# Kernel tuning notes

Measured on AMD Instinct MI355X. Metric: run time of the kernel, lower is better.

Reference implementation:

```python
import jax, jax.numpy as jnp
import numpy as np

B, T, I = 32, 512, 96
H, M, R, K = 256, 6, 16, 16
TASK, SENS = 32, 64
MPG = M // 3  # mechanisms per group
OUT = 64


def setup_inputs() -> dict:
    key = jax.random.key(0)
    ks = jax.random.split(key, 12)
    inp = {
        'x': jax.random.normal(ks[0], (B, T, I), jnp.float32),
        # stacked per-mechanism LowRankRNNCell params
        'W_ip': jax.random.normal(ks[1], (M, H, H), jnp.float32) / np.sqrt(H),
        'b_ip': jnp.zeros((M, H), jnp.float32),
        'U': jax.random.normal(ks[2], (M, H, R), jnp.float32) / np.sqrt(R),
        'Vr': jax.random.normal(ks[3], (M, R, H), jnp.float32) / np.sqrt(H),
        'cell_bias': jnp.zeros((M, H), jnp.float32),
        'W_in_task': 0.01 * jax.random.normal(ks[4], (MPG, TASK, H), jnp.float32),
        'W_in_sensory': 0.01 * jax.random.normal(ks[5], (MPG, SENS, H), jnp.float32),
        'W_Q': 0.01 * jax.random.normal(ks[6], (M, H, K), jnp.float32),
        'W_K': 0.01 * jax.random.normal(ks[7], (M, H, K), jnp.float32),
        'W_V': 0.01 * jax.random.normal(ks[8], (M, H, H), jnp.float32),
        'W_out': jax.random.normal(ks[9], (H * MPG, OUT), jnp.float32) / np.sqrt(H * MPG),
        'b_out': jnp.zeros((OUT,), jnp.float32),
    }
    return inp


def _rim_forward(x, W_ip, b_ip, U, Vr, cell_bias, W_in_task, W_in_sensory,
                 W_Q, W_K, W_V, W_out, b_out):
    scale = jnp.float32(1.0 / np.sqrt(K))

    def step(Hs, x_t):
        # input routing: group 0 <- task input, group 1 <- sensory, group 2 <- zeros
        x_task = x_t[:, -TASK:]
        x_sens = x_t[:, :-TASK]
        g0 = jnp.einsum('bi,mih->bmh', x_task, W_in_task)
        g1 = jnp.einsum('bi,mih->bmh', x_sens, W_in_sensory)
        A_in = jnp.concatenate([g0, g1, jnp.zeros_like(g0)], axis=1)  # [B,M,H]
        # batched LowRankRNNCell update per mechanism
        inp_part = jnp.einsum('bmi,mih->bmh', A_in, W_ip) + b_ip
        rec = jnp.einsum('bmr,mrh->bmh', jnp.einsum('bmh,mhr->bmr', Hs, U), Vr)
        H_in = jnp.tanh(inp_part + rec + cell_bias)  # [B,M,H]
        # communication attention (exact einsum structure of the original)
        Qc = jnp.einsum('bmh,mhk->bmk', H_in, W_Q)
        Kc = jnp.einsum('bmh,mhk->bmk', H_in, W_K)
        Vc = jnp.einsum('bmh,mhj->bjm', H_in, W_V)  # V_comm[b,h,m]
        attn = jax.nn.softmax(jnp.einsum('bmk,bnk->bmn', Qc, Kc) * scale, axis=-1)
        A_comm = jnp.einsum('bmn,bhm->bnh', attn, Vc)
        H_new = H_in + A_comm
        out = H_new[:, -MPG:].reshape(H_new.shape[0], -1) @ W_out + b_out
        return H_new, (out, H_new, A_in, A_comm, attn)

    H0 = jnp.zeros((x.shape[0], M, H), x.dtype)
    _, (outs, Hseq, Ain_seq, Acomm_seq, attn_seq) = jax.lax.scan(
        step, H0, jnp.swapaxes(x, 0, 1))
    # time-major -> batch-major where the torch code stacks on dim=1 (outputs)
    outputs = jnp.swapaxes(outs, 0, 1)  # [B,T,OUT]
    return outputs, Hseq, Ain_seq, Acomm_seq, attn_seq


def reference(x, W_ip, b_ip, U, Vr, cell_bias, W_in_task, W_in_sensory,
              W_Q, W_K, W_V, W_out, b_out):
    return _rim_forward(x, W_ip, b_ip, U, Vr, cell_bias, W_in_task,
                        W_in_sensory, W_Q, W_K, W_V, W_out, b_out)
```

## Files before the change

### kernel.cpp

```cpp
#include <hip/hip_runtime.h>
#include <math.h>

#define BB 32
#define TT 512
#define II 96
#define HH 256
#define MM 6
#define OUTD 64

#define O_HSEQ  1048576
#define O_AIN   26214400
#define O_ACM   51380224
#define O_ATTN  76546048

#define WS_WEFF 0
#define WS_UT   49152
#define WS_WQT  73728
#define WS_WKT  98304
#define WS_VCH  122880
#define WS_QK   319488
#define WS_FLAG 331776
#define WS_COOP_FLOATS 333824

#define LBAR() asm volatile("s_waitcnt lgkmcnt(0)\n\ts_barrier" ::: "memory")

__global__ __launch_bounds__(256) void rim_weff(
    const float* __restrict__ Wtask, const float* __restrict__ Wsens,
    const float* __restrict__ Wip,
    const float* __restrict__ U, const float* __restrict__ WQ, const float* __restrict__ WK,
    float* __restrict__ Weff, float* __restrict__ Ut, float* __restrict__ WQt, float* __restrict__ WKt)
{
  __shared__ float row[256];
  const int bidx = blockIdx.x;
  const int tid = threadIdx.x;
  if (bidx < 192) {
    int m, i;
    if (bidx < 32)       { m = 0; i = bidx; }
    else if (bidx < 64)  { m = 1; i = bidx - 32; }
    else if (bidx < 128) { m = 2; i = bidx - 64; }
    else                 { m = 3; i = bidx - 128; }
    row[tid] = (m < 2) ? Wtask[(m * 32 + i) * 256 + tid]
                       : Wsens[((m - 2) * 64 + i) * 256 + tid];
    __syncthreads();
    float acc = 0.f;
    const float* wip = Wip + m * 65536 + tid;
    #pragma unroll 8
    for (int j = 0; j < 256; ++j) acc += row[j] * wip[j * 256];
    const int base = (m == 0) ? 0 : (m == 1) ? 8192 : (m == 2) ? 16384 : 32768;
    Weff[base + i * 256 + tid] = acc;
  } else {
    const int p = bidx - 192;
    const int m = p >> 4, r = p & 15;
    Ut [(m * 16 + r) * 256 + tid] = U [m * 4096 + tid * 16 + r];
    WQt[(m * 16 + r) * 256 + tid] = WQ[m * 4096 + tid * 16 + r];
    WKt[(m * 16 + r) * 256 + tid] = WK[m * 4096 + tid * 16 + r];
  }
}

__global__ __launch_bounds__(256) void rim_pre(
    const float* __restrict__ x,
    const float* __restrict__ Wtask, const float* __restrict__ Wsens,
    float* __restrict__ Ain)
{
  __shared__ float xr[16][96];
  const int tid = threadIdx.x;
  const int rb0 = blockIdx.x * 16;
  for (int idx = tid; idx < 16 * 96; idx += 256) {
    int r = idx / 96, c = idx % 96;
    int rb = rb0 + r; int t = rb >> 5, b = rb & 31;
    xr[r][c] = x[(b * TT + t) * II + c];
  }
  __syncthreads();
  const int h = tid;
  float acc[16];

  for (int m = 0; m < 4; ++m) {
    const int cnt  = (m < 2) ? 32 : 64;
    const int xoff = (m < 2) ? 64 : 0;
    const float* W = (m < 2) ? (Wtask + m * 32 * 256) : (Wsens + (m - 2) * 64 * 256);
    #pragma unroll
    for (int r = 0; r < 16; ++r) acc[r] = 0.f;
    for (int i = 0; i < cnt; ++i) {
      float w = W[i * 256 + h];
      #pragma unroll
      for (int r = 0; r < 16; ++r) acc[r] += xr[r][xoff + i] * w;
    }
    #pragma unroll
    for (int r = 0; r < 16; ++r) {
      int rb = rb0 + r; int t = rb >> 5, b = rb & 31;
      Ain[((t * 32 + b) * 6 + m) * 256 + h] = acc[r];
    }
  }
  #pragma unroll
  for (int r = 0; r < 16; ++r) {
    int rb = rb0 + r; int t = rb >> 5, b = rb & 31;
    Ain[((t * 32 + b) * 6 + 4) * 256 + h] = 0.f;
    Ain[((t * 32 + b) * 6 + 5) * 256 + h] = 0.f;
  }
}

__global__ __launch_bounds__(512, 2) void rim_step(
    const float* __restrict__ x,
    const float* __restrict__ Vr, const float* __restrict__ WV,
    const float* __restrict__ bip, const float* __restrict__ cbias,
    const float* __restrict__ UtW, const float* __restrict__ WQtW,
    const float* __restrict__ WKtW, const float* __restrict__ WeffW,
    float* __restrict__ VcHG, float* __restrict__ QKG,
    unsigned int* __restrict__ seqG,
    float* __restrict__ Hseq, float* __restrict__ Acm, float* __restrict__ attnO)
{
  __shared__ __align__(16) float Hl[256];
  __shared__ __align__(16) float Hin[256];
  __shared__ float biasl[256];
  __shared__ float Utl[16][257];
  __shared__ float Vrl[16][257];
  __shared__ float WQtl[16][257];
  __shared__ float WKtl[16][257];
  __shared__ float Weffl[64][256];
  __shared__ float inpl[2][256];
  __shared__ float xl[2][96];
  __shared__ float tmpUr[16];
  __shared__ float qklw[4][192];

  const int bid = blockIdx.x;
  const int m = bid >> 5;
  const int b = bid & 31;
  const int tid = threadIdx.x;
  const int g32 = tid >> 5, l32 = tid & 31;
  const int h_out = tid & 255, p = tid >> 8;
  const int g16 = tid >> 4, l16 = tid & 15;
  const int w64 = tid >> 6, lane = tid & 63;

  const int base = (m == 0) ? 0 : (m == 1) ? 8192 : (m == 2) ? 16384 : 32768;
  const int cnt  = (m < 2) ? 32 : 64;
  const int xoff = (m < 2) ? 64 : 0;

  for (int i = tid; i < 4096; i += 512) {
    int r = i >> 8, c = i & 255;
    Utl [r][c] = UtW [m * 4096 + i];
    Vrl [r][c] = Vr  [m * 4096 + i];
    WQtl[r][c] = WQtW[m * 4096 + i];
    WKtl[r][c] = WKtW[m * 4096 + i];
  }
  if (m < 4)
    for (int i = tid; i < cnt * 256; i += 512)
      ((float*)Weffl)[i] = WeffW[base + i];
  if (tid < 256) {
    biasl[tid] = bip[m * 256 + tid] + cbias[m * 256 + tid];
    Hl[tid] = 0.f;
  }
  float xreg = 0.f;
  if (m < 4 && tid < 96) {
    xl[0][tid] = x[((size_t)b * TT + 0) * II + tid];
    xreg       = x[((size_t)b * TT + 1) * II + tid];
  }
  float w[128];
  #pragma unroll
  for (int j = 0; j < 128; ++j)
    w[j] = WV[((size_t)(m * 256 + p * 128 + j)) * 256 + h_out];
  __syncthreads();
  if (m < 4 && tid < 256) {
    float a = 0.f;
    for (int i = 0; i < cnt; ++i) a += xl[0][xoff + i] * Weffl[i][tid];
    inpl[0][tid] = a;
  }
  __syncthreads();

  for (int t = 0; t < TT; ++t) {
    const int buf = t & 1;
    const int mb12 = (buf * 32 + b) * 12;
    const int qb   = (buf * 32 + b) * 192;
    const unsigned target = (unsigned)(t + 1);

    if (m < 4 && tid < 96) {
      xl[(t + 1) & 1][tid] = xreg;
      xreg = (t + 2 < TT) ? x[((size_t)b * TT + t + 2) * II + tid] : 0.f;
    }

    {
      float s = 0.f;
      const float* up = &Utl[g32][0];
      #pragma unroll
      for (int h = l32; h < 256; h += 32) s += Hl[h] * up[h];
      #pragma unroll
      for (int off = 16; off > 0; off >>= 1) s += __shfl_down(s, off, 32);
      if (l32 == 0) tmpUr[g32] = s;
    }
    LBAR();

    if (tid < 256) {
      float rec = 0.f;
      #pragma unroll
      for (int r = 0; r < 16; ++r) rec += tmpUr[r] * Vrl[r][tid];
      float inp = (m < 4) ? inpl[buf][tid] : 0.f;
      Hin[tid] = tanhf(inp + rec + biasl[tid]);
    }
    LBAR();

    {
      const int r = g16 & 15;
      const float* wp = (g16 < 16) ? &WQtl[r][0] : &WKtl[r][0];
      float s = 0.f;
      #pragma unroll
      for (int j = 0; j < 16; ++j) { int h = l16 + 16 * j; s += Hin[h] * wp[h]; }
      s += __shfl_down(s, 8, 16);
      s += __shfl_down(s, 4, 16);
      s += __shfl_down(s, 2, 16);
      s += __shfl_down(s, 1, 16);
      if (l16 == 0)
        __hip_atomic_store(&QKG[qb + ((g16 < 16) ? 0 : 96) + m * 16 + r], s,
                           __ATOMIC_RELAXED, __HIP_MEMORY_SCOPE_SYSTEM);
    }
    float accVc = 0.f;
    {
      const float4* h4 = (const float4*)&Hin[p * 128];
      #pragma unroll
      for (int q = 0; q < 32; ++q) {
        float4 hv = h4[q];
        accVc += hv.x * w[4 * q] + hv.y * w[4 * q + 1]
               + hv.z * w[4 * q + 2] + hv.w * w[4 * q + 3];
      }
      __hip_atomic_store(&VcHG[(mb12 + m * 2 + p) * 256 + h_out], accVc,
                         __ATOMIC_RELAXED, __HIP_MEMORY_SCOPE_SYSTEM);
    }
    asm volatile("s_waitcnt vmcnt(0)" ::: "memory");
    if (lane == 0)
      __hip_atomic_store(&seqG[b * 64 + m * 8 + w64], target,
                         __ATOMIC_RELAXED, __HIP_MEMORY_SCOPE_SYSTEM);

    if (w64 < 4) {
      if (lane < 48) {
        while (__hip_atomic_load(&seqG[b * 64 + lane],
                                 __ATOMIC_RELAXED, __HIP_MEMORY_SCOPE_SYSTEM)
               < target) { }
      }
      float q0 = __hip_atomic_load(&QKG[qb + lane],       __ATOMIC_RELAXED, __HIP_MEMORY_SCOPE_SYSTEM);
      float q1 = __hip_atomic_load(&QKG[qb + 64 + lane],  __ATOMIC_RELAXED, __HIP_MEMORY_SCOPE_SYSTEM);
      float q2 = __hip_atomic_load(&QKG[qb + 128 + lane], __ATOMIC_RELAXED, __HIP_MEMORY_SCOPE_SYSTEM);
      float vA[6], vB[6];
      #pragma unroll
      for (int mm = 0; mm < 6; ++mm) {
        if (mm != m)
          vA[mm] = __hip_atomic_load(&VcHG[(mb12 + mm * 2 + 0) * 256 + h_out],
                                     __ATOMIC_RELAXED, __HIP_MEMORY_SCOPE_SYSTEM);
        vB[mm] = __hip_atomic_load(&VcHG[(mb12 + mm * 2 + 1) * 256 + h_out],
                                   __ATOMIC_RELAXED, __HIP_MEMORY_SCOPE_SYSTEM);
      }
      vA[m] = accVc;

      qklw[w64][lane]       = q0;
      qklw[w64][64 + lane]  = q1;
      qklw[w64][128 + lane] = q2;

      float a = 0.f;
      {
        const int mm6 = (lane < 36) ? (lane / 6) : 0;
        const int nn  = (lane < 36) ? (lane % 6) : 0;
        if (lane < 36) {
          const float* qw = &qklw[w64][mm6 * 16];
          const float* kw = &qklw[w64][96 + nn * 16];
          float s = 0.f;
          #pragma unroll
          for (int k = 0; k < 16; ++k) s += qw[k] * kw[k];
          s *= 0.25f;
          float mx = s;
          #pragma unroll
          for (int d = 1; d < 6; ++d)
            mx = fmaxf(mx, __shfl(s, mm6 * 6 + ((nn + d) % 6), 64));
          float e = __expf(s - mx);
          float sm = e;
          #pragma unroll
          for (int d = 1; d < 6; ++d)
            sm += __shfl(e, mm6 * 6 + ((nn + d) % 6), 64);
          a = e / sm;
        }
      }
      if (m == 0 && w64 == 0 && lane < 36)
        attnO[((size_t)t * 32 + b) * 36 + lane] = a;

      float ac = 0.f;
      #pragma unroll
      for (int mm = 0; mm < 6; ++mm) {
        float amm = __shfl(a, mm * 6 + m, 64);
        ac += amm * (vA[mm] + vB[mm]);
      }
      float hn = Hin[tid] + ac;
      Hl[tid] = hn;
      size_t gi = (((size_t)t * 32 + b) * 6 + m) * 256 + tid;
      Hseq[gi] = hn;
      Acm[gi]  = ac;
    } else {
      if (m < 4) {
        const int h = tid - 256, nb = (t + 1) & 1;
        float a = 0.f;
        for (int i = 0; i < cnt; ++i) a += xl[nb][xoff + i] * Weffl[i][h];
        inpl[nb][h] = a;
      }
    }
    LBAR();
  }
}

__global__ __launch_bounds__(256) void rim_out(
    const float* __restrict__ Hseq, const float* __restrict__ Wout,
    const float* __restrict__ bout, float* __restrict__ out0)
{
  __shared__ float hrow[4][512];
  const int tid = threadIdx.x;
  const int row0 = blockIdx.x * 4;
  for (int i = tid; i < 4 * 512; i += 256) {
    int r = i >> 9, j = i & 511;
    int rb = row0 + r; int b = rb >> 9, t = rb & 511;
    hrow[r][j] = Hseq[((size_t)(t * 32 + b) * 6 + 4 + (j >> 8)) * 256 + (j & 255)];
  }
  __syncthreads();
  const int r = tid >> 6, o = tid & 63;
  const int rb = row0 + r;
  float s = bout[o];
  const float* hp = hrow[r];
  const float* wp = Wout + o;
  #pragma unroll 8
  for (int j = 0; j < 512; ++j) s += hp[j] * wp[(size_t)j * 64];
  out0[(size_t)rb * 64 + o] = s;
}

__global__ __launch_bounds__(512) void rim_loop(
    const float* __restrict__ x,
    const float* __restrict__ Vr, const float* __restrict__ WV,
    const float* __restrict__ Wout, const float* __restrict__ bout,
    const float* __restrict__ bip, const float* __restrict__ cbias,
    const float* __restrict__ Ut, const float* __restrict__ WQt, const float* __restrict__ WKt,
    const float* __restrict__ Weff,
    float* __restrict__ out0, float* __restrict__ Hseq,
    float* __restrict__ Acm, float* __restrict__ attnO)
{
  __shared__ float Hl[6][256];
  __shared__ float Hin[6][256];
  __shared__ float biasl[6][256];
  __shared__ float Vcp[2][6][256];
  __shared__ float tmpUr[6][16];
  __shared__ float Qc[6][16], Kc[6][16];
  __shared__ float attnl[36];
  __shared__ float pout[8][64];
  __shared__ float xl[96];
  __shared__ float inpl[4][256];

  const int b = blockIdx.x;
  const int tid = threadIdx.x;
  const int wid = tid >> 5, lane = tid & 31;

  for (int i = tid; i < 1536; i += 512) {
    int m = i >> 8, h = i & 255;
    biasl[m][h] = bip[i] + cbias[i];
    Hl[m][h] = 0.f;
  }
  __syncthreads();

  for (int t = 0; t < TT; ++t) {
    if (tid < 96) xl[tid] = x[(b * TT + t) * II + tid];
    __syncthreads();
    for (int mh = tid; mh < 1024; mh += 512) {
      int m = mh >> 8, h = mh & 255;
      const int base = (m == 0) ? 0 : (m == 1) ? 8192 : (m == 2) ? 16384 : 32768;
      const int cnt  = (m < 2) ? 32 : 64;
      const int xoff = (m < 2) ? 64 : 0;
      float a = 0.f;
      for (int i = 0; i < cnt; ++i) a += xl[xoff + i] * Weff[base + i * 256 + h];
      inpl[m][h] = a;
    }

    for (int pq = wid; pq < 96; pq += 16) {
      int m = pq >> 4, r = pq & 15;
      const float* up = Ut + (m * 16 + r) * 256;
      float s = 0.f;
      #pragma unroll
      for (int h = lane; h < 256; h += 32) s += Hl[m][h] * up[h];
// ... 68 lines not shown
      #pragma unroll
      for (int m = 0; m < 6; ++m)
        ac += attnl[m * 6 + n] * (Vcp[0][m][h] + Vcp[1][m][h]);
      float hn = Hin[n][h] + ac;
      Hl[n][h] = hn;
      size_t gi = ((size_t)(t * 32 + b) * 6 + n) * 256 + h;
      Hseq[gi] = hn;
      Acm[gi]  = ac;
    }
    __syncthreads();

    {
      const int o = tid & 63, js = tid >> 6;
      const float* hp = &Hl[4][0];
      const float* wp = Wout + (size_t)(js * 64) * 64 + o;
      float s = 0.f;
      #pragma unroll 8
      for (int jj = 0; jj < 64; ++jj) s += hp[js * 64 + jj] * wp[(size_t)jj * 64];
      pout[js][o] = s;
    }
    __syncthreads();
    if (tid < 64) {
      float s = bout[tid];
      #pragma unroll
      for (int js = 0; js < 8; ++js) s += pout[js][tid];
      out0[(size_t)(b * TT + t) * 64 + tid] = s;
    }
  }
}

extern "C" void kernel_launch(void* const* d_in, const int* in_sizes, int n_in,
                              void* d_out, int out_size, void* d_ws, size_t ws_size,
                              hipStream_t stream) {
  const float* x    = (const float*)d_in[0];
  const float* W_ip = (const float*)d_in[1];
  const float* b_ip = (const float*)d_in[2];
  const float* U    = (const float*)d_in[3];
  const float* Vr   = (const float*)d_in[4];
  const float* cb   = (const float*)d_in[5];
  const float* Wt   = (const float*)d_in[6];
  const float* Wsn  = (const float*)d_in[7];
  const float* WQ   = (const float*)d_in[8];
  const float* WK   = (const float*)d_in[9];
  const float* WV   = (const float*)d_in[10];
  const float* Wo   = (const float*)d_in[11];
  const float* bo   = (const float*)d_in[12];

  float* out  = (float*)d_out;
  float* Hseq = out + O_HSEQ;
  float* Ain  = out + O_AIN;
  float* Acm  = out + O_ACM;
  float* attn = out + O_ATTN;

  float* ws   = (float*)d_ws;
  float* Weff = ws + WS_WEFF;
  float* Ut   = ws + WS_UT;
  float* WQt  = ws + WS_WQT;
  float* WKt  = ws + WS_WKT;

  hipLaunchKernelGGL(rim_weff, dim3(288), dim3(256), 0, stream,
                     Wt, Wsn, W_ip, U, WQ, WK, Weff, Ut, WQt, WKt);
  hipLaunchKernelGGL(rim_pre, dim3(1024), dim3(256), 0, stream,
                     x, Wt, Wsn, Ain);

  if (ws_size >= (size_t)WS_COOP_FLOATS * sizeof(float)) {
    float* VcHG = ws + WS_VCH;
    float* QKG  = ws + WS_QK;
    unsigned int* seqG = (unsigned int*)(ws + WS_FLAG);
    hipMemsetAsync((void*)seqG, 0, 2048 * sizeof(unsigned int), stream);

    void* args[] = { (void*)&x, (void*)&Vr, (void*)&WV, (void*)&b_ip, (void*)&cb,
                     (void*)&Ut, (void*)&WQt, (void*)&WKt, (void*)&Weff,
                     (void*)&VcHG, (void*)&QKG, (void*)&seqG,
                     (void*)&Hseq, (void*)&Acm, (void*)&attn };
    hipLaunchCooperativeKernel((void*)rim_step, dim3(192), dim3(512), args, 0, stream);

    hipLaunchKernelGGL(rim_out, dim3(4096), dim3(256), 0, stream,
                       Hseq, Wo, bo, out);
  } else {
    hipLaunchKernelGGL(rim_loop, dim3(32), dim3(512), 0, stream,
                       x, Vr, WV, Wo, bo, b_ip, cb, Ut, WQt, WKt, Weff,
                       out, Hseq, Acm, attn);
  }
}
```

Baseline: 3.162 ms.

## Replace per-step flag barrier with tagged value exchange and fuse weight prep

Inter-block communication in the cooperative recurrent kernel now packs each value with its timestep tag into a 64-bit word. Consumers spin directly on the data instead of on a separate sequence-flag array after a vmcnt drain. The Vc partial sums are combined in LDS before publishing, and a dedicated wavefront computes the softmax once per block. The Weff and transposed-weight precompute kernel is folded into the step kernel's prologue, removing one launch but making every block redo the W_ip product. The aim is shorter per-timestep synchronization latency, at the cost of doubled exchange traffic and a heavier prologue.

```diff
diff --git a/kernel.cpp b/kernel.cpp
--- a/kernel.cpp
+++ b/kernel.cpp
@@ -1,28 +1,320 @@
 #include <hip/hip_runtime.h>
 #include <math.h>
+
+typedef unsigned long long u64;
 
 #define BB 32
 #define TT 512
 #define II 96
-#define HH 256
-#define MM 6
-#define OUTD 64
 
 #define O_HSEQ  1048576
 #define O_AIN   26214400
 #define O_ACM   51380224
 #define O_ATTN  76546048
 
-#define WS_WEFF 0
-#define WS_UT   49152
-#define WS_WQT  73728
-#define WS_WKT  98304
-#define WS_VCH  122880
-#define WS_QK   319488
-#define WS_FLAG 331776
-#define WS_COOP_FLOATS 333824
+#define WS_VCF  0
+#define WS_QKT  196608
+#define WS_COOP_FLOATS 221184
+#define WS_F_WEFF 0
+#define WS_F_UT   49152
+#define WS_F_WQT  73728
+#define WS_F_WKT  98304
+#define WS_F_FLOATS 122880
 
 #define LBAR() asm volatile("s_waitcnt lgkmcnt(0)\n\ts_barrier" ::: "memory")
+
+__device__ __forceinline__ u64 sysld(const u64* p) {
+  return __hip_atomic_load(p, __ATOMIC_RELAXED, __HIP_MEMORY_SCOPE_SYSTEM);
+}
+__device__ __forceinline__ void sysst(u64* p, u64 v) {
+  __hip_atomic_store(p, v, __ATOMIC_RELAXED, __HIP_MEMORY_SCOPE_SYSTEM);
+}
+__device__ __forceinline__ u64 packtv(unsigned tag, float v) {
+  return ((u64)tag << 32) | (u64)__float_as_uint(v);
+}
+
+__global__ __launch_bounds__(256) void rim_pre(
+    const float* __restrict__ x,
+    const float* __restrict__ Wtask, const float* __restrict__ Wsens,
+    float* __restrict__ Ain)
+{
+  __shared__ float xr[16][96];
+  const int tid = threadIdx.x;
+  const int rb0 = blockIdx.x * 16;
+  for (int idx = tid; idx < 16 * 96; idx += 256) {
+    int r = idx / 96, c = idx % 96;
+    int rb = rb0 + r; int t = rb >> 5, b = rb & 31;
+    xr[r][c] = x[(b * TT + t) * II + c];
+  }
+  __syncthreads();
+  const int h = tid;
+  float acc[16];
+
+  for (int m = 0; m < 4; ++m) {
+    const int cnt  = (m < 2) ? 32 : 64;
+    const int xoff = (m < 2) ? 64 : 0;
+    const float* W = (m < 2) ? (Wtask + m * 32 * 256) : (Wsens + (m - 2) * 64 * 256);
+    #pragma unroll
+    for (int r = 0; r < 16; ++r) acc[r] = 0.f;
+    for (int i = 0; i < cnt; ++i) {
+      float w = W[i * 256 + h];
+      #pragma unroll
+      for (int r = 0; r < 16; ++r) acc[r] += xr[r][xoff + i] * w;
+    }
+    #pragma unroll
+    for (int r = 0; r < 16; ++r) {
+      int rb = rb0 + r; int t = rb >> 5, b = rb & 31;
+      Ain[((t * 32 + b) * 6 + m) * 256 + h] = acc[r];
+    }
+  }
+  #pragma unroll
+  for (int r = 0; r < 16; ++r) {
+    int rb = rb0 + r; int t = rb >> 5, b = rb & 31;
+    Ain[((t * 32 + b) * 6 + 4) * 256 + h] = 0.f;
+    Ain[((t * 32 + b) * 6 + 5) * 256 + h] = 0.f;
+  }
+}
+
+__global__ __launch_bounds__(512, 1) void rim_step(
+    const float* __restrict__ x,
+    const float* __restrict__ U, const float* __restrict__ Vr,
+    const float* __restrict__ WV,
+    const float* __restrict__ bip, const float* __restrict__ cbias,
+    const float* __restrict__ WQ, const float* __restrict__ WK,
+    const float* __restrict__ Wtask, const float* __restrict__ Wsens,
+    const float* __restrict__ Wip,
+    u64* __restrict__ VCF, u64* __restrict__ QKT,
+    float* __restrict__ Hseq, float* __restrict__ Acm, float* __restrict__ attnO)
+{
+  __shared__ __align__(16) float Hl[256];
+  __shared__ __align__(16) float Hin[256];
+  __shared__ float biasl[256];
+  __shared__ float Utl[16][257];
+  __shared__ float Vrl[16][257];
+  __shared__ float WQtl[16][257];
+  __shared__ float WKtl[16][257];
+  __shared__ float Weffl[64][256];
+  __shared__ float inpl[2][256];
+  __shared__ float xl[2][96];
+  __shared__ float Vcp1[256];
+  __shared__ float tmpUr[16];
+  __shared__ float attnl[40];
+  __shared__ float qkl[192];
+  __shared__ float wtmp[16][256];
+
+  const int bid = blockIdx.x;
+  const int m = bid >> 5;
+  const int b = bid & 31;
+  const int tid = threadIdx.x;
+  const int g32 = tid >> 5, l32 = tid & 31;
+  const int h_out = tid & 255, p = tid >> 8;
+  const int g16 = tid >> 4, l16 = tid & 15;
+  const int w64 = tid >> 6, lane = tid & 63;
+
+  const int cnt  = (m < 2) ? 32 : 64;
+  const int xoff = (m < 2) ? 64 : 0;
+
+  for (int i = tid; i < 4096; i += 512) {
+    int r = i >> 8, c = i & 255;
+    Utl [r][c] = U [m * 4096 + c * 16 + r];
+    WQtl[r][c] = WQ[m * 4096 + c * 16 + r];
+    WKtl[r][c] = WK[m * 4096 + c * 16 + r];
+    Vrl [r][c] = Vr[m * 4096 + i];
+  }
+  if (tid < 256) {
+    biasl[tid] = bip[m * 256 + tid] + cbias[m * 256 + tid];
+    Hl[tid] = 0.f;
+  }
+  float xreg = 0.f;
+  if (m < 4 && tid < 96) {
+    xl[0][tid] = x[((size_t)b * TT + 0) * II + tid];
+    xreg       = x[((size_t)b * TT + 1) * II + tid];
+  }
+  float w[128];
+  #pragma unroll
+  for (int j = 0; j < 128; ++j)
+    w[j] = WV[((size_t)(m * 256 + p * 128 + j)) * 256 + h_out];
+
+  if (m < 4) {
+    const float* Win = (m < 2) ? (Wtask + m * 32 * 256) : (Wsens + (m - 2) * 64 * 256);
+    const float* wip = Wip + m * 65536;
+    const int hh = tid & 255, half8 = (tid >> 8) * 8;
+    for (int c0 = 0; c0 < cnt; c0 += 16) {
+      __syncthreads();
+      for (int i = tid; i < 16 * 256; i += 512)
+        wtmp[i >> 8][i & 255] = Win[(c0 + (i >> 8)) * 256 + (i & 255)];
+      __syncthreads();
+      float acc8[8];
+      #pragma unroll
+      for (int r = 0; r < 8; ++r) acc8[r] = 0.f;
+      for (int j = 0; j < 256; ++j) {
+        float wv = wip[j * 256 + hh];
+        #pragma unroll
+        for (int r = 0; r < 8; ++r) acc8[r] += wtmp[half8 + r][j] * wv;
+      }
+      #pragma unroll
+      for (int r = 0; r < 8; ++r) Weffl[c0 + half8 + r][hh] = acc8[r];
+    }
+  }
+  __syncthreads();
+  if (m < 4 && tid < 256) {
+    float a = 0.f;
+    for (int i = 0; i < cnt; ++i) a += xl[0][xoff + i] * Weffl[i][tid];
+    inpl[0][tid] = a;
+  }
+  __syncthreads();
+
+  for (int t = 0; t < TT; ++t) {
+    const int buf = t & 1;
+    const unsigned target = (unsigned)(t + 1);
+    u64* vcb = VCF + (size_t)(buf * 32 + b) * 1536;
+    u64* qkb = QKT + (size_t)(buf * 32 + b) * 192;
+
+    if (m < 4 && tid < 96) {
+      xl[(t + 1) & 1][tid] = xreg;
+      xreg = (t + 2 < TT) ? x[((size_t)b * TT + t + 2) * II + tid] : 0.f;
+    }
+
+    {
+      float s = 0.f;
+      const float* up = &Utl[g32][0];
+      #pragma unroll
+      for (int h = l32; h < 256; h += 32) s += Hl[h] * up[h];
+      #pragma unroll
+      for (int off = 16; off > 0; off >>= 1) s += __shfl_down(s, off, 32);
+      if (l32 == 0) tmpUr[g32] = s;
+    }
+    LBAR();
+
+    if (tid < 256) {
+      float rec = 0.f;
+      #pragma unroll
+      for (int r = 0; r < 16; ++r) rec += tmpUr[r] * Vrl[r][tid];
+      float inp = (m < 4) ? inpl[buf][tid] : 0.f;
+      Hin[tid] = tanhf(inp + rec + biasl[tid]);
+    }
+    LBAR();
+
+    {
+      const int r = g16 & 15;
+      const float* wp = (g16 < 16) ? &WQtl[r][0] : &WKtl[r][0];
+      float s = 0.f;
+      #pragma unroll
+      for (int j = 0; j < 16; ++j) { int h = l16 + 16 * j; s += Hin[h] * wp[h]; }
+      s += __shfl_down(s, 8, 16);
+      s += __shfl_down(s, 4, 16);
+      s += __shfl_down(s, 2, 16);
+      s += __shfl_down(s, 1, 16);
+      if (l16 == 0)
+        sysst(&qkb[((g16 < 16) ? 0 : 96) + m * 16 + r], packtv(target, s));
+    }
+    float accVc = 0.f;
+    {
+      const float4* h4 = (const float4*)&Hin[p * 128];
+      #pragma unroll
+      for (int q = 0; q < 32; ++q) {
+        float4 hv = h4[q];
+        accVc += hv.x * w[4 * q] + hv.y * w[4 * q + 1]
+               + hv.z * w[4 * q + 2] + hv.w * w[4 * q + 3];
+      }
+    }
+    if (p == 1) Vcp1[h_out] = accVc;
+    LBAR();
+
+    float vC[6];
+    if (tid < 256) {
+      float vown = accVc + Vcp1[tid];
+      sysst(&vcb[m * 256 + tid], packtv(target, vown));
+      u64 vw[6];
+      #pragma unroll
+      for (int mm = 0; mm < 6; ++mm)
+        if (mm != m) vw[mm] = sysld(&vcb[mm * 256 + tid]);
+      #pragma unroll
+      for (int mm = 0; mm < 6; ++mm)
+        if (mm != m)
+          while ((unsigned)(vw[mm] >> 32) != target)
+            vw[mm] = sysld(&vcb[mm * 256 + tid]);
+      #pragma unroll
+      for (int mm = 0; mm < 6; ++mm)
+        vC[mm] = (mm == m) ? vown : __uint_as_float((unsigned)vw[mm]);
+    } else if (w64 == 7) {
+      u64 a0 = sysld(&qkb[lane]);
+      u64 a1 = sysld(&qkb[64 + lane]);
+      u64 a2 = sysld(&qkb[128 + lane]);
+      while ((unsigned)(a0 >> 32) != target) a0 = sysld(&qkb[lane]);
+      while ((unsigned)(a1 >> 32) != target) a1 = sysld(&qkb[64 + lane]);
+      while ((unsigned)(a2 >> 32) != target) a2 = sysld(&qkb[128 + lane]);
+      qkl[lane]       = __uint_as_float((unsigned)a0);
+      qkl[64 + lane]  = __uint_as_float((unsigned)a1);
+      qkl[128 + lane] = __uint_as_float((unsigned)a2);
+      asm volatile("s_waitcnt lgkmcnt(0)" ::: "memory");
+      if (lane < 36) {
+        const int mm6 = lane / 6, nn = lane % 6;
+        float s = 0.f;
+        #pragma unroll
+        for (int k = 0; k < 16; ++k) s += qkl[mm6 * 16 + k] * qkl[96 + nn * 16 + k];
+        s *= 0.25f;
+        float mx = s;
+        #pragma unroll
+        for (int d = 1; d < 6; ++d)
+          mx = fmaxf(mx, __shfl(s, mm6 * 6 + ((nn + d) % 6), 64));
+        float e = __expf(s - mx);
+        float sm = e;
+        #pragma unroll
+        for (int d = 1; d < 6; ++d)
+          sm += __shfl(e, mm6 * 6 + ((nn + d) % 6), 64);
+        float a = e / sm;
+        attnl[lane] = a;
+        if (m == 0) attnO[((size_t)t * 32 + b) * 36 + lane] = a;
+      }
+    } else {
+      if (m < 4) {
+        const int nb = (t + 1) & 1;
+        for (int h = tid - 256; h < 256; h += 192) {
+          float a = 0.f;
+          for (int i = 0; i < cnt; ++i) a += xl[nb][xoff + i] * Weffl[i][h];
+          inpl[nb][h] = a;
+        }
+      }
+    }
+    LBAR();
+
+    if (tid < 256) {
+      float ac = 0.f;
+      #pragma unroll
+      for (int mm = 0; mm < 6; ++mm) ac += attnl[mm * 6 + m] * vC[mm];
+      float hn = Hin[tid] + ac;
+      Hl[tid] = hn;
+      size_t gi = (((size_t)t * 32 + b) * 6 + m) * 256 + tid;
+      Hseq[gi] = hn;
+      Acm[gi]  = ac;
+    }
+    LBAR();
+  }
+}
+
+__global__ __launch_bounds__(256) void rim_out(
+    const float* __restrict__ Hseq, const float* __restrict__ Wout,
+    const float* __restrict__ bout, float* __restrict__ out0)
+{
+  __shared__ float hrow[4][512];
+  const int tid = threadIdx.x;
+  const int row0 = blockIdx.x * 4;
+  for (int i = tid; i < 4 * 512; i += 256) {
+    int r = i >> 9, j = i & 511;
+    int rb = row0 + r; int b = rb >> 9, t = rb & 511;
+    hrow[r][j] = Hseq[((size_t)(t * 32 + b) * 6 + 4 + (j >> 8)) * 256 + (j & 255)];
+  }
+  __syncthreads();
+  const int r = tid >> 6, o = tid & 63;
+  const int rb = row0 + r;
+  float s = bout[o];
+  const float* hp = hrow[r];
+  const float* wp = Wout + o;
+  #pragma unroll 8
+  for (int j = 0; j < 512; ++j) s += hp[j] * wp[(size_t)j * 64];
+  out0[(size_t)rb * 64 + o] = s;
+}
 
 __global__ __launch_bounds__(256) void rim_weff(
     const float* __restrict__ Wtask, const float* __restrict__ Wsens,
@@ -55,273 +347,6 @@
     WQt[(m * 16 + r) * 256 + tid] = WQ[m * 4096 + tid * 16 + r];
     WKt[(m * 16 + r) * 256 + tid] = WK[m * 4096 + tid * 16 + r];
   }
-}
-
-__global__ __launch_bounds__(256) void rim_pre(
-    const float* __restrict__ x,
-    const float* __restrict__ Wtask, const float* __restrict__ Wsens,
-    float* __restrict__ Ain)
-{
-  __shared__ float xr[16][96];
-  const int tid = threadIdx.x;
-  const int rb0 = blockIdx.x * 16;
-  for (int idx = tid; idx < 16 * 96; idx += 256) {
-    int r = idx / 96, c = idx % 96;
-    int rb = rb0 + r; int t = rb >> 5, b = rb & 31;
-    xr[r][c] = x[(b * TT + t) * II + c];
-  }
-  __syncthreads();
-  const int h = tid;
-  float acc[16];
-
-  for (int m = 0; m < 4; ++m) {
-    const int cnt  = (m < 2) ? 32 : 64;
-    const int xoff = (m < 2) ? 64 : 0;
-    const float* W = (m < 2) ? (Wtask + m * 32 * 256) : (Wsens + (m - 2) * 64 * 256);
-    #pragma unroll
-    for (int r = 0; r < 16; ++r) acc[r] = 0.f;
-    for (int i = 0; i < cnt; ++i) {
-      float w = W[i * 256 + h];
-      #pragma unroll
-      for (int r = 0; r < 16; ++r) acc[r] += xr[r][xoff + i] * w;
-    }
-    #pragma unroll
-    for (int r = 0; r < 16; ++r) {
-      int rb = rb0 + r; int t = rb >> 5, b = rb & 31;
-      Ain[((t * 32 + b) * 6 + m) * 256 + h] = acc[r];
-    }
-  }
-  #pragma unroll
-  for (int r = 0; r < 16; ++r) {
-    int rb = rb0 + r; int t = rb >> 5, b = rb & 31;
-    Ain[((t * 32 + b) * 6 + 4) * 256 + h] = 0.f;
-    Ain[((t * 32 + b) * 6 + 5) * 256 + h] = 0.f;
-  }
-}
-
-__global__ __launch_bounds__(512, 2) void rim_step(
-    const float* __restrict__ x,
-    const float* __restrict__ Vr, const float* __restrict__ WV,
-    const float* __restrict__ bip, const float* __restrict__ cbias,
-    const float* __restrict__ UtW, const float* __restrict__ WQtW,
-    const float* __restrict__ WKtW, const float* __restrict__ WeffW,
-    float* __restrict__ VcHG, float* __restrict__ QKG,
-    unsigned int* __restrict__ seqG,
-    float* __restrict__ Hseq, float* __restrict__ Acm, float* __restrict__ attnO)
-{
-  __shared__ __align__(16) float Hl[256];
-  __shared__ __align__(16) float Hin[256];
-  __shared__ float biasl[256];
-  __shared__ float Utl[16][257];
-  __shared__ float Vrl[16][257];
-  __shared__ float WQtl[16][257];
-  __shared__ float WKtl[16][257];
-  __shared__ float Weffl[64][256];
-  __shared__ float inpl[2][256];
-  __shared__ float xl[2][96];
-  __shared__ float tmpUr[16];
-  __shared__ float qklw[4][192];
-
-  const int bid = blockIdx.x;
-  const int m = bid >> 5;
-  const int b = bid & 31;
-  const int tid = threadIdx.x;
-  const int g32 = tid >> 5, l32 = tid & 31;
-  const int h_out = tid & 255, p = tid >> 8;
-  const int g16 = tid >> 4, l16 = tid & 15;
-  const int w64 = tid >> 6, lane = tid & 63;
-
-  const int base = (m == 0) ? 0 : (m == 1) ? 8192 : (m == 2) ? 16384 : 32768;
-  const int cnt  = (m < 2) ? 32 : 64;
-  const int xoff = (m < 2) ? 64 : 0;
-
-  for (int i = tid; i < 4096; i += 512) {
-    int r = i >> 8, c = i & 255;
-    Utl [r][c] = UtW [m * 4096 + i];
-    Vrl [r][c] = Vr  [m * 4096 + i];
-    WQtl[r][c] = WQtW[m * 4096 + i];
-    WKtl[r][c] = WKtW[m * 4096 + i];
-  }
-  if (m < 4)
-    for (int i = tid; i < cnt * 256; i += 512)
-      ((float*)Weffl)[i] = WeffW[base + i];
-  if (tid < 256) {
-    biasl[tid] = bip[m * 256 + tid] + cbias[m * 256 + tid];
-    Hl[tid] = 0.f;
-  }
-  float xreg = 0.f;
-  if (m < 4 && tid < 96) {
-    xl[0][tid] = x[((size_t)b * TT + 0) * II + tid];
-    xreg       = x[((size_t)b * TT + 1) * II + tid];
-  }
-  float w[128];
-  #pragma unroll
-  for (int j = 0; j < 128; ++j)
-    w[j] = WV[((size_t)(m * 256 + p * 128 + j)) * 256 + h_out];
-  __syncthreads();
-  if (m < 4 && tid < 256) {
-    float a = 0.f;
-    for (int i = 0; i < cnt; ++i) a += xl[0][xoff + i] * Weffl[i][tid];
-    inpl[0][tid] = a;
-  }
-  __syncthreads();
-
-  for (int t = 0; t < TT; ++t) {
-    const int buf = t & 1;
-    const int mb12 = (buf * 32 + b) * 12;
-    const int qb   = (buf * 32 + b) * 192;
-    const unsigned target = (unsigned)(t + 1);
-
-    if (m < 4 && tid < 96) {
-      xl[(t + 1) & 1][tid] = xreg;
-      xreg = (t + 2 < TT) ? x[((size_t)b * TT + t + 2) * II + tid] : 0.f;
-    }
-
-    {
-      float s = 0.f;
-      const float* up = &Utl[g32][0];
-      #pragma unroll
-      for (int h = l32; h < 256; h += 32) s += Hl[h] * up[h];
-      #pragma unroll
-      for (int off = 16; off > 0; off >>= 1) s += __shfl_down(s, off, 32);
-      if (l32 == 0) tmpUr[g32] = s;
-    }
-    LBAR();
-
-    if (tid < 256) {
-      float rec = 0.f;
-      #pragma unroll
-      for (int r = 0; r < 16; ++r) rec += tmpUr[r] * Vrl[r][tid];
-      float inp = (m < 4) ? inpl[buf][tid] : 0.f;
-      Hin[tid] = tanhf(inp + rec + biasl[tid]);
-    }
-    LBAR();
-
-    {
-      const int r = g16 & 15;
-      const float* wp = (g16 < 16) ? &WQtl[r][0] : &WKtl[r][0];
-      float s = 0.f;
-      #pragma unroll
-      for (int j = 0; j < 16; ++j) { int h = l16 + 16 * j; s += Hin[h] * wp[h]; }
-      s += __shfl_down(s, 8, 16);
-      s += __shfl_down(s, 4, 16);
-      s += __shfl_down(s, 2, 16);
-      s += __shfl_down(s, 1, 16);
-      if (l16 == 0)
-        __hip_atomic_store(&QKG[qb + ((g16 < 16) ? 0 : 96) + m * 16 + r], s,
-                           __ATOMIC_RELAXED, __HIP_MEMORY_SCOPE_SYSTEM);
-    }
-    float accVc = 0.f;
-    {
-      const float4* h4 = (const float4*)&Hin[p * 128];
-      #pragma unroll
-      for (int q = 0; q < 32; ++q) {
-        float4 hv = h4[q];
-        accVc += hv.x * w[4 * q] + hv.y * w[4 * q + 1]
-               + hv.z * w[4 * q + 2] + hv.w * w[4 * q + 3];
-      }
-      __hip_atomic_store(&VcHG[(mb12 + m * 2 + p) * 256 + h_out], accVc,
-                         __ATOMIC_RELAXED, __HIP_MEMORY_SCOPE_SYSTEM);
-    }
-    asm volatile("s_waitcnt vmcnt(0)" ::: "memory");
-    if (lane == 0)
-      __hip_atomic_store(&seqG[b * 64 + m * 8 + w64], target,
-                         __ATOMIC_RELAXED, __HIP_MEMORY_SCOPE_SYSTEM);
-
-    if (w64 < 4) {
-      if (lane < 48) {
-        while (__hip_atomic_load(&seqG[b * 64 + lane],
-                                 __ATOMIC_RELAXED, __HIP_MEMORY_SCOPE_SYSTEM)
-               < target) { }
-      }
-      float q0 = __hip_atomic_load(&QKG[qb + lane],       __ATOMIC_RELAXED, __HIP_MEMORY_SCOPE_SYSTEM);
-      float q1 = __hip_atomic_load(&QKG[qb + 64 + lane],  __ATOMIC_RELAXED, __HIP_MEMORY_SCOPE_SYSTEM);
-      float q2 = __hip_atomic_load(&QKG[qb + 128 + lane], __ATOMIC_RELAXED, __HIP_MEMORY_SCOPE_SYSTEM);
-      float vA[6], vB[6];
-      #pragma unroll
-      for (int mm = 0; mm < 6; ++mm) {
-        if (mm != m)
-          vA[mm] = __hip_atomic_load(&VcHG[(mb12 + mm * 2 + 0) * 256 + h_out],
-                                     __ATOMIC_RELAXED, __HIP_MEMORY_SCOPE_SYSTEM);
-        vB[mm] = __hip_atomic_load(&VcHG[(mb12 + mm * 2 + 1) * 256 + h_out],
-                                   __ATOMIC_RELAXED, __HIP_MEMORY_SCOPE_SYSTEM);
-      }
-      vA[m] = accVc;
-
-      qklw[w64][lane]       = q0;
-      qklw[w64][64 + lane]  = q1;
-      qklw[w64][128 + lane] = q2;
-
-      float a = 0.f;
-      {
-        const int mm6 = (lane < 36) ? (lane / 6) : 0;
-        const int nn  = (lane < 36) ? (lane % 6) : 0;
-        if (lane < 36) {
-          const float* qw = &qklw[w64][mm6 * 16];
-          const float* kw = &qklw[w64][96 + nn * 16];
-          float s = 0.f;
-          #pragma unroll
-          for (int k = 0; k < 16; ++k) s += qw[k] * kw[k];
-          s *= 0.25f;
-          float mx = s;
-          #pragma unroll
-          for (int d = 1; d < 6; ++d)
-            mx = fmaxf(mx, __shfl(s, mm6 * 6 + ((nn + d) % 6), 64));
-          float e = __expf(s - mx);
-          float sm = e;
-          #pragma unroll
-          for (int d = 1; d < 6; ++d)
-            sm += __shfl(e, mm6 * 6 + ((nn + d) % 6), 64);
-          a = e / sm;
-        }
-      }
-      if (m == 0 && w64 == 0 && lane < 36)
-        attnO[((size_t)t * 32 + b) * 36 + lane] = a;
-
-      float ac = 0.f;
-      #pragma unroll
-      for (int mm = 0; mm < 6; ++mm) {
-        float amm = __shfl(a, mm * 6 + m, 64);
-        ac += amm * (vA[mm] + vB[mm]);
-      }
-      float hn = Hin[tid] + ac;
-      Hl[tid] = hn;
-      size_t gi = (((size_t)t * 32 + b) * 6 + m) * 256 + tid;
-      Hseq[gi] = hn;
-      Acm[gi]  = ac;
-    } else {
-      if (m < 4) {
-        const int h = tid - 256, nb = (t + 1) & 1;
-        float a = 0.f;
-        for (int i = 0; i < cnt; ++i) a += xl[nb][xoff + i] * Weffl[i][h];
-        inpl[nb][h] = a;
-      }
-    }
-    LBAR();
-  }
-}
-
-__global__ __launch_bounds__(256) void rim_out(
-    const float* __restrict__ Hseq, const float* __restrict__ Wout,
-    const float* __restrict__ bout, float* __restrict__ out0)
-{
-  __shared__ float hrow[4][512];
-  const int tid = threadIdx.x;
-  const int row0 = blockIdx.x * 4;
-  for (int i = tid; i < 4 * 512; i += 256) {
-    int r = i >> 9, j = i & 511;
-    int rb = row0 + r; int b = rb >> 9, t = rb & 511;
-    hrow[r][j] = Hseq[((size_t)(t * 32 + b) * 6 + 4 + (j >> 8)) * 256 + (j & 255)];
-  }
-  __syncthreads();
-  const int r = tid >> 6, o = tid & 63;
-  const int rb = row0 + r;
-  float s = bout[o];
-  const float* hp = hrow[r];
-  const float* wp = Wout + o;
-  #pragma unroll 8
-  for (int j = 0; j < 512; ++j) s += hp[j] * wp[(size_t)j * 64];
-  out0[(size_t)rb * 64 + o] = s;
 }
 
 __global__ __launch_bounds__(512) void rim_loop(
@@ -496,32 +521,32 @@
   float* Acm  = out + O_ACM;
   float* attn = out + O_ATTN;
 
-  float* ws   = (float*)d_ws;
-  float* Weff = ws + WS_WEFF;
-  float* Ut   = ws + WS_UT;
-  float* WQt  = ws + WS_WQT;
-  float* WKt  = ws + WS_WKT;
-
-  hipLaunchKernelGGL(rim_weff, dim3(288), dim3(256), 0, stream,
-                     Wt, Wsn, W_ip, U, WQ, WK, Weff, Ut, WQt, WKt);
+  float* ws = (float*)d_ws;
+
   hipLaunchKernelGGL(rim_pre, dim3(1024), dim3(256), 0, stream,
                      x, Wt, Wsn, Ain);
 
   if (ws_size >= (size_t)WS_COOP_FLOATS * sizeof(float)) {
-    float* VcHG = ws + WS_VCH;
-    float* QKG  = ws + WS_QK;
-    unsigned int* seqG = (unsigned int*)(ws + WS_FLAG);
-    hipMemsetAsync((void*)seqG, 0, 2048 * sizeof(unsigned int), stream);
-
-    void* args[] = { (void*)&x, (void*)&Vr, (void*)&WV, (void*)&b_ip, (void*)&cb,
-                     (void*)&Ut, (void*)&WQt, (void*)&WKt, (void*)&Weff,
-                     (void*)&VcHG, (void*)&QKG, (void*)&seqG,
+    u64* VCF = (u64*)(ws + WS_VCF);
+    u64* QKT = (u64*)(ws + WS_QKT);
+    hipMemsetAsync((void*)ws, 0, (size_t)WS_COOP_FLOATS * sizeof(float), stream);
+
+    void* args[] = { (void*)&x, (void*)&U, (void*)&Vr, (void*)&WV,
+                     (void*)&b_ip, (void*)&cb, (void*)&WQ, (void*)&WK,
+                     (void*)&Wt, (void*)&Wsn, (void*)&W_ip,
+                     (void*)&VCF, (void*)&QKT,
                      (void*)&Hseq, (void*)&Acm, (void*)&attn };
     hipLaunchCooperativeKernel((void*)rim_step, dim3(192), dim3(512), args, 0, stream);
 
     hipLaunchKernelGGL(rim_out, dim3(4096), dim3(256), 0, stream,
                        Hseq, Wo, bo, out);
   } else {
+    float* Weff = ws + WS_F_WEFF;
+    float* Ut   = ws + WS_F_UT;
+    float* WQt  = ws + WS_F_WQT;
+    float* WKt  = ws + WS_F_WKT;
+    hipLaunchKernelGGL(rim_weff, dim3(288), dim3(256), 0, stream,
+                       Wt, Wsn, W_ip, U, WQ, WK, Weff, Ut, WQt, WKt);
     hipLaunchKernelGGL(rim_loop, dim3(32), dim3(512), 0, stream,
                        x, Vr, WV, Wo, bo, b_ip, cb, Ut, WQt, WKt, Weff,
                        out, Hseq, Acm, attn);
```

After: 3.966 ms. 25.4% more time.

## Batch four sequences per block in cooperative RIM step kernel

Applied to the files above, without the earlier changes.

Each block of the cooperative recurrent kernel now handles one mechanism for four batch elements instead of one, shrinking the grid from 192 to 48 blocks. The two halves of the V projection are summed locally before publishing, which halves cross-block Vc traffic. Cross-block flag synchronization drops to one flag per block and six pollers per step. The trade-off is that each block runs four serialized sub-steps with extra barriers per timestep and uses fewer CUs, in exchange for cheaper inter-block synchronization.

```diff
diff --git a/kernel.cpp b/kernel.cpp
--- a/kernel.cpp
+++ b/kernel.cpp
@@ -4,9 +4,6 @@
 #define BB 32
 #define TT 512
 #define II 96
-#define HH 256
-#define MM 6
-#define OUTD 64
 
 #define O_HSEQ  1048576
 #define O_AIN   26214400
@@ -17,12 +14,25 @@
 #define WS_UT   49152
 #define WS_WQT  73728
 #define WS_WKT  98304
-#define WS_VCH  122880
-#define WS_QK   319488
-#define WS_FLAG 331776
-#define WS_COOP_FLOATS 333824
+#define WS_VC   122880
+#define WS_QK   221184
+#define WS_FLAG 233472
+#define WS_COOP_FLOATS 233728
 
 #define LBAR() asm volatile("s_waitcnt lgkmcnt(0)\n\ts_barrier" ::: "memory")
+
+__device__ __forceinline__ float sysldf(const float* p) {
+  return __hip_atomic_load(p, __ATOMIC_RELAXED, __HIP_MEMORY_SCOPE_SYSTEM);
+}
+__device__ __forceinline__ void sysstf(float* p, float v) {
+  __hip_atomic_store(p, v, __ATOMIC_RELAXED, __HIP_MEMORY_SCOPE_SYSTEM);
+}
+__device__ __forceinline__ unsigned sysld32(const unsigned* p) {
+  return __hip_atomic_load(p, __ATOMIC_RELAXED, __HIP_MEMORY_SCOPE_SYSTEM);
+}
+__device__ __forceinline__ void sysst32(unsigned* p, unsigned v) {
+  __hip_atomic_store(p, v, __ATOMIC_RELAXED, __HIP_MEMORY_SCOPE_SYSTEM);
+}
 
 __global__ __launch_bounds__(256) void rim_weff(
     const float* __restrict__ Wtask, const float* __restrict__ Wsens,
@@ -105,35 +115,38 @@
     const float* __restrict__ bip, const float* __restrict__ cbias,
     const float* __restrict__ UtW, const float* __restrict__ WQtW,
     const float* __restrict__ WKtW, const float* __restrict__ WeffW,
-    float* __restrict__ VcHG, float* __restrict__ QKG,
-    unsigned int* __restrict__ seqG,
+    float* __restrict__ VcG, float* __restrict__ QKG,
+    unsigned* __restrict__ seqG,
     float* __restrict__ Hseq, float* __restrict__ Acm, float* __restrict__ attnO)
 {
-  __shared__ __align__(16) float Hl[256];
-  __shared__ __align__(16) float Hin[256];
+  __shared__ float Hl[4][256];
+  __shared__ float Hin[4][256];
+  __shared__ float inpl[4][2][256];
+  __shared__ float xl[4][2][96];
+  __shared__ float qkl[4][192];
+  __shared__ float attnl[4][40];
   __shared__ float biasl[256];
-  __shared__ float Utl[16][257];
-  __shared__ float Vrl[16][257];
+  __shared__ float Vcp1[256];
+  __shared__ float tmpUr[16];
+  __shared__ float Utl[16][256];
+  __shared__ float Vrl[16][256];
   __shared__ float WQtl[16][257];
   __shared__ float WKtl[16][257];
   __shared__ float Weffl[64][256];
-  __shared__ float inpl[2][256];
-  __shared__ float xl[2][96];
-  __shared__ float tmpUr[16];
-  __shared__ float qklw[4][192];
 
   const int bid = blockIdx.x;
-  const int m = bid >> 5;
-  const int b = bid & 31;
+  const int m  = bid >> 3;
+  const int g  = bid & 7;
+  const int b0 = g * 4;
   const int tid = threadIdx.x;
   const int g32 = tid >> 5, l32 = tid & 31;
-  const int h_out = tid & 255, p = tid >> 8;
   const int g16 = tid >> 4, l16 = tid & 15;
   const int w64 = tid >> 6, lane = tid & 63;
-
-  const int base = (m == 0) ? 0 : (m == 1) ? 8192 : (m == 2) ? 16384 : 32768;
+  const int h_out = tid & 255, p = tid >> 8;
+
   const int cnt  = (m < 2) ? 32 : 64;
   const int xoff = (m < 2) ? 64 : 0;
+  const int wbase = (m == 0) ? 0 : (m == 1) ? 8192 : (m == 2) ? 16384 : 32768;
 
   for (int i = tid; i < 4096; i += 512) {
     int r = i >> 8, c = i & 255;
@@ -144,15 +157,15 @@
   }
   if (m < 4)
     for (int i = tid; i < cnt * 256; i += 512)
-      ((float*)Weffl)[i] = WeffW[base + i];
-  if (tid < 256) {
-    biasl[tid] = bip[m * 256 + tid] + cbias[m * 256 + tid];
-    Hl[tid] = 0.f;
-  }
+      ((float*)Weffl)[i] = WeffW[wbase + i];
+  if (tid < 256) biasl[tid] = bip[m * 256 + tid] + cbias[m * 256 + tid];
+  for (int i = tid; i < 1024; i += 512) Hl[i >> 8][i & 255] = 0.f;
+
   float xreg = 0.f;
-  if (m < 4 && tid < 96) {
-    xl[0][tid] = x[((size_t)b * TT + 0) * II + tid];
-    xreg       = x[((size_t)b * TT + 1) * II + tid];
+  if (m < 4 && tid < 384) {
+    const int bi = tid / 96, c = tid % 96;
+    xl[bi][0][c] = x[((size_t)(b0 + bi) * TT + 0) * II + c];
+    xreg         = x[((size_t)(b0 + bi) * TT + 1) * II + c];
   }
   float w[128];
   #pragma unroll
@@ -160,141 +173,153 @@
     w[j] = WV[((size_t)(m * 256 + p * 128 + j)) * 256 + h_out];
   __syncthreads();
   if (m < 4 && tid < 256) {
-    float a = 0.f;
-    for (int i = 0; i < cnt; ++i) a += xl[0][xoff + i] * Weffl[i][tid];
-    inpl[0][tid] = a;
+    #pragma unroll
+    for (int bi = 0; bi < 4; ++bi) {
+      float a = 0.f;
+      for (int i = 0; i < cnt; ++i) a += xl[bi][0][xoff + i] * Weffl[i][tid];
+      inpl[bi][0][tid] = a;
+    }
   }
   __syncthreads();
 
+  float accVcS[4];
   for (int t = 0; t < TT; ++t) {
-    const int buf = t & 1;
-    const int mb12 = (buf * 32 + b) * 12;
-    const int qb   = (buf * 32 + b) * 192;
+    const int buf = t & 1, nb = buf ^ 1;
     const unsigned target = (unsigned)(t + 1);
-
-    if (m < 4 && tid < 96) {
-      xl[(t + 1) & 1][tid] = xreg;
-      xreg = (t + 2 < TT) ? x[((size_t)b * TT + t + 2) * II + tid] : 0.f;
-    }
-
-    {
+    const int vcbase = (buf * 32 + b0) * 1536;
+    const int qkbase = (buf * 32 + b0) * 192;
+
+    if (m < 4 && tid < 384) {
+      const int bi = tid / 96, c = tid % 96;
+      xl[bi][nb][c] = xreg;
+      xreg = (t + 2 < TT) ? x[((size_t)(b0 + bi) * TT + t + 2) * II + c] : 0.f;
+    }
+
+    #pragma unroll
+    for (int bi = 0; bi < 4; ++bi) {
+      if (bi > 0 && tid < 256)
+        sysstf(&VcG[vcbase + (bi - 1) * 1536 + m * 256 + tid],
+               accVcS[bi - 1] + Vcp1[tid]);
+      {
+        float s = 0.f;
+        const float* up = &Utl[g32][0];
+        const float* hp = &Hl[bi][0];
+        #pragma unroll
+        for (int h = l32; h < 256; h += 32) s += hp[h] * up[h];
+        #pragma unroll
+        for (int off = 16; off; off >>= 1) s += __shfl_down(s, off, 32);
+        if (l32 == 0) tmpUr[g32] = s;
+      }
+      LBAR();
+      if (tid < 256) {
+        float rec = 0.f;
+        #pragma unroll
+        for (int r = 0; r < 16; ++r) rec += tmpUr[r] * Vrl[r][tid];
+        float inp = (m < 4) ? inpl[bi][buf][tid] : 0.f;
+        Hin[bi][tid] = tanhf(inp + rec + biasl[tid]);
+      }
+      LBAR();
+      {
+        const int r = g16 & 15;
+        const float* wp = (g16 < 16) ? &WQtl[r][0] : &WKtl[r][0];
+        const float* hp = &Hin[bi][0];
+        float s = 0.f;
+        #pragma unroll
+        for (int j = 0; j < 16; ++j) { int h = l16 + 16 * j; s += hp[h] * wp[h]; }
+        s += __shfl_down(s, 8, 16);
+        s += __shfl_down(s, 4, 16);
+        s += __shfl_down(s, 2, 16);
+        s += __shfl_down(s, 1, 16);
+        if (l16 == 0)
+          sysstf(&QKG[qkbase + bi * 192 + ((g16 < 16) ? 0 : 96) + m * 16 + r], s);
+      }
+      {
+        float acc = 0.f;
+        const float4* h4 = (const float4*)&Hin[bi][p * 128];
+        #pragma unroll
+        for (int q = 0; q < 32; ++q) {
+          float4 hv = h4[q];
+          acc += hv.x * w[4 * q] + hv.y * w[4 * q + 1]
+               + hv.z * w[4 * q + 2] + hv.w * w[4 * q + 3];
+        }
+        accVcS[bi] = acc;
+        if (p == 1) Vcp1[h_out] = acc;
+      }
+      LBAR();
+    }
+    if (tid < 256)
+      sysstf(&VcG[vcbase + 3 * 1536 + m * 256 + tid], accVcS[3] + Vcp1[tid]);
+
+    asm volatile("s_waitcnt vmcnt(0)" ::: "memory");
+    LBAR();
+    if (tid == 0) sysst32(&seqG[m * 8 + g], target);
+    if (w64 == 0 && lane < 6)
+      while (sysld32(&seqG[lane * 8 + g]) < target) { }
+    LBAR();
+
+    float vA[4][6];
+    if (tid < 256) {
+      #pragma unroll
+      for (int bi = 0; bi < 4; ++bi)
+        #pragma unroll
+        for (int mm = 0; mm < 6; ++mm)
+          vA[bi][mm] = sysldf(&VcG[vcbase + bi * 1536 + mm * 256 + tid]);
+    } else {
+      const int f0 = (tid - 256) * 3;
+      float q0 = sysldf(&QKG[qkbase + f0]);
+      float q1 = sysldf(&QKG[qkbase + f0 + 1]);
+      float q2 = sysldf(&QKG[qkbase + f0 + 2]);
+      if (m < 4) {
+        const int h = tid - 256;
+        #pragma unroll
+        for (int bi = 0; bi < 4; ++bi) {
+          float a = 0.f;
+          for (int i = 0; i < cnt; ++i) a += xl[bi][nb][xoff + i] * Weffl[i][h];
+          inpl[bi][nb][h] = a;
+        }
+      }
+      ((float*)qkl)[f0]     = q0;
+      ((float*)qkl)[f0 + 1] = q1;
+      ((float*)qkl)[f0 + 2] = q2;
+    }
+    LBAR();
+
+    if (w64 >= 4 && lane < 36) {
+      const int bi = w64 - 4;
+      const int mm6 = lane / 6, nn = lane % 6;
+      const float* qw = &qkl[bi][mm6 * 16];
+      const float* kw = &qkl[bi][96 + nn * 16];
       float s = 0.f;
-      const float* up = &Utl[g32][0];
-      #pragma unroll
-      for (int h = l32; h < 256; h += 32) s += Hl[h] * up[h];
-      #pragma unroll
-      for (int off = 16; off > 0; off >>= 1) s += __shfl_down(s, off, 32);
-      if (l32 == 0) tmpUr[g32] = s;
+      #pragma unroll
+      for (int k = 0; k < 16; ++k) s += qw[k] * kw[k];
+      s *= 0.25f;
+      float mx = s;
+      #pragma unroll
+      for (int d = 1; d < 6; ++d)
+        mx = fmaxf(mx, __shfl(s, mm6 * 6 + ((nn + d) % 6), 64));
+      float e = __expf(s - mx);
+      float sm = e;
+      #pragma unroll
+      for (int d = 1; d < 6; ++d)
+        sm += __shfl(e, mm6 * 6 + ((nn + d) % 6), 64);
+      float a = e / sm;
+      attnl[bi][lane] = a;
+      if (m == 0) attnO[((size_t)t * 32 + (b0 + bi)) * 36 + lane] = a;
     }
     LBAR();
 
     if (tid < 256) {
-      float rec = 0.f;
-      #pragma unroll
-      for (int r = 0; r < 16; ++r) rec += tmpUr[r] * Vrl[r][tid];
-      float inp = (m < 4) ? inpl[buf][tid] : 0.f;
-      Hin[tid] = tanhf(inp + rec + biasl[tid]);
-    }
-    LBAR();
-
-    {
-      const int r = g16 & 15;
-      const float* wp = (g16 < 16) ? &WQtl[r][0] : &WKtl[r][0];
-      float s = 0.f;
-      #pragma unroll
-      for (int j = 0; j < 16; ++j) { int h = l16 + 16 * j; s += Hin[h] * wp[h]; }
-      s += __shfl_down(s, 8, 16);
-      s += __shfl_down(s, 4, 16);
-      s += __shfl_down(s, 2, 16);
-      s += __shfl_down(s, 1, 16);
-      if (l16 == 0)
-        __hip_atomic_store(&QKG[qb + ((g16 < 16) ? 0 : 96) + m * 16 + r], s,
-                           __ATOMIC_RELAXED, __HIP_MEMORY_SCOPE_SYSTEM);
-    }
-    float accVc = 0.f;
-    {
-      const float4* h4 = (const float4*)&Hin[p * 128];
-      #pragma unroll
-      for (int q = 0; q < 32; ++q) {
-        float4 hv = h4[q];
-        accVc += hv.x * w[4 * q] + hv.y * w[4 * q + 1]
-               + hv.z * w[4 * q + 2] + hv.w * w[4 * q + 3];
-      }
-      __hip_atomic_store(&VcHG[(mb12 + m * 2 + p) * 256 + h_out], accVc,
-                         __ATOMIC_RELAXED, __HIP_MEMORY_SCOPE_SYSTEM);
-    }
-    asm volatile("s_waitcnt vmcnt(0)" ::: "memory");
-    if (lane == 0)
-      __hip_atomic_store(&seqG[b * 64 + m * 8 + w64], target,
-                         __ATOMIC_RELAXED, __HIP_MEMORY_SCOPE_SYSTEM);
-
-    if (w64 < 4) {
-      if (lane < 48) {
-        while (__hip_atomic_load(&seqG[b * 64 + lane],
-                                 __ATOMIC_RELAXED, __HIP_MEMORY_SCOPE_SYSTEM)
-               < target) { }
-      }
-      float q0 = __hip_atomic_load(&QKG[qb + lane],       __ATOMIC_RELAXED, __HIP_MEMORY_SCOPE_SYSTEM);
-      float q1 = __hip_atomic_load(&QKG[qb + 64 + lane],  __ATOMIC_RELAXED, __HIP_MEMORY_SCOPE_SYSTEM);
-      float q2 = __hip_atomic_load(&QKG[qb + 128 + lane], __ATOMIC_RELAXED, __HIP_MEMORY_SCOPE_SYSTEM);
-      float vA[6], vB[6];
-      #pragma unroll
-      for (int mm = 0; mm < 6; ++mm) {
-        if (mm != m)
-          vA[mm] = __hip_atomic_load(&VcHG[(mb12 + mm * 2 + 0) * 256 + h_out],
-                                     __ATOMIC_RELAXED, __HIP_MEMORY_SCOPE_SYSTEM);
-        vB[mm] = __hip_atomic_load(&VcHG[(mb12 + mm * 2 + 1) * 256 + h_out],
-                                   __ATOMIC_RELAXED, __HIP_MEMORY_SCOPE_SYSTEM);
-      }
-      vA[m] = accVc;
-
-      qklw[w64][lane]       = q0;
-      qklw[w64][64 + lane]  = q1;
-      qklw[w64][128 + lane] = q2;
-
-      float a = 0.f;
-      {
-        const int mm6 = (lane < 36) ? (lane / 6) : 0;
-        const int nn  = (lane < 36) ? (lane % 6) : 0;
-        if (lane < 36) {
-          const float* qw = &qklw[w64][mm6 * 16];
-          const float* kw = &qklw[w64][96 + nn * 16];
-          float s = 0.f;
-          #pragma unroll
-          for (int k = 0; k < 16; ++k) s += qw[k] * kw[k];
-          s *= 0.25f;
-          float mx = s;
-          #pragma unroll
-          for (int d = 1; d < 6; ++d)
-            mx = fmaxf(mx, __shfl(s, mm6 * 6 + ((nn + d) % 6), 64));
-          float e = __expf(s - mx);
-          float sm = e;
-          #pragma unroll
-          for (int d = 1; d < 6; ++d)
-            sm += __shfl(e, mm6 * 6 + ((nn + d) % 6), 64);
-          a = e / sm;
-        }
-      }
-      if (m == 0 && w64 == 0 && lane < 36)
-        attnO[((size_t)t * 32 + b) * 36 + lane] = a;
-
-      float ac = 0.f;
-      #pragma unroll
-      for (int mm = 0; mm < 6; ++mm) {
-        float amm = __shfl(a, mm * 6 + m, 64);
-        ac += amm * (vA[mm] + vB[mm]);
-      }
-      float hn = Hin[tid] + ac;
-      Hl[tid] = hn;
-      size_t gi = (((size_t)t * 32 + b) * 6 + m) * 256 + tid;
-      Hseq[gi] = hn;
-      Acm[gi]  = ac;
-    } else {
-      if (m < 4) {
-        const int h = tid - 256, nb = (t + 1) & 1;
-        float a = 0.f;
-        for (int i = 0; i < cnt; ++i) a += xl[nb][xoff + i] * Weffl[i][h];
-        inpl[nb][h] = a;
+      #pragma unroll
+      for (int bi = 0; bi < 4; ++bi) {
+        float ac = 0.f;
+        #pragma unroll
+        for (int mm = 0; mm < 6; ++mm)
+          ac += attnl[bi][mm * 6 + m] * vA[bi][mm];
+        float hn = Hin[bi][tid] + ac;
+        Hl[bi][tid] = hn;
+        size_t gi = (((size_t)t * 32 + (b0 + bi)) * 6 + m) * 256 + tid;
+        Hseq[gi] = hn;
+        Acm[gi]  = ac;
       }
     }
     LBAR();
@@ -508,16 +533,16 @@
                      x, Wt, Wsn, Ain);
 
   if (ws_size >= (size_t)WS_COOP_FLOATS * sizeof(float)) {
-    float* VcHG = ws + WS_VCH;
-    float* QKG  = ws + WS_QK;
-    unsigned int* seqG = (unsigned int*)(ws + WS_FLAG);
-    hipMemsetAsync((void*)seqG, 0, 2048 * sizeof(unsigned int), stream);
+    float* VcG = ws + WS_VC;
+    float* QKG = ws + WS_QK;
+    unsigned* seqG = (unsigned*)(ws + WS_FLAG);
+    hipMemsetAsync((void*)seqG, 0, 256 * sizeof(unsigned), stream);
 
     void* args[] = { (void*)&x, (void*)&Vr, (void*)&WV, (void*)&b_ip, (void*)&cb,
                      (void*)&Ut, (void*)&WQt, (void*)&WKt, (void*)&Weff,
-                     (void*)&VcHG, (void*)&QKG, (void*)&seqG,
+                     (void*)&VcG, (void*)&QKG, (void*)&seqG,
                      (void*)&Hseq, (void*)&Acm, (void*)&attn };
-    hipLaunchCooperativeKernel((void*)rim_step, dim3(192), dim3(512), args, 0, stream);
+    hipLaunchCooperativeKernel((void*)rim_step, dim3(48), dim3(512), args, 0, stream);
 
     hipLaunchKernelGGL(rim_out, dim3(4096), dim3(256), 0, stream,
                        Hseq, Wo, bo, out);
```

Result: slower. 6.188 ms (+95.7%).
